# Kernel tuning notes

Hardware: AMD Instinct MI355X
Metric: run time of the kernel (lower is better)

The kernel has to match this reference:

```python
import jax, jax.numpy as jnp
import numpy as np

NUM_HEADS = 16
HEAD_DIM = 64
D_MODEL = NUM_HEADS * HEAD_DIM
DFF = 4096
LN_EPS = 1e-3  # keras LayerNormalization default epsilon


def layer_norm(x, gamma, beta):
    mu = jnp.mean(x, axis=-1, keepdims=True)
    var = jnp.mean(jnp.square(x - mu), axis=-1, keepdims=True)
    return (x - mu) * jax.lax.rsqrt(var + LN_EPS) * gamma + beta


def setup_inputs() -> dict:
    key = jax.random.key(0)
    ks = jax.random.split(key, 8)
    N, T = 2, 2048
    s = 0.02
    return {
        "x": jax.random.normal(ks[0], (N, T, D_MODEL), dtype=jnp.float32),
        "mask": jnp.ones((N, T), dtype=jnp.float32),
        "w_qkv": jax.random.normal(ks[1], (D_MODEL, 3 * D_MODEL), dtype=jnp.float32) * s,
        "b_qkv": jnp.zeros((3 * D_MODEL,), dtype=jnp.float32),
        "w_ff": jax.random.normal(ks[2], (D_MODEL, DFF), dtype=jnp.float32) * s,
        "b_ff": jnp.zeros((DFF,), dtype=jnp.float32),
        "w_out": jax.random.normal(ks[3], (DFF, D_MODEL), dtype=jnp.float32) * s,
        "b_out": jnp.zeros((D_MODEL,), dtype=jnp.float32),
        "ln1_g": jnp.ones((D_MODEL,), dtype=jnp.float32),
        "ln1_b": jnp.zeros((D_MODEL,), dtype=jnp.float32),
        "ln2_g": jnp.ones((D_MODEL,), dtype=jnp.float32),
        "ln2_b": jnp.zeros((D_MODEL,), dtype=jnp.float32),
    }


def reference(x, mask, w_qkv, b_qkv, w_ff, b_ff, w_out, b_out, ln1_g, ln1_b, ln2_g, ln2_b):
    N, T, _ = x.shape
    H, D = NUM_HEADS, HEAD_DIM
    # --- MHA ---
    qkv = x @ w_qkv + b_qkv                     # [N, T, 3*H*D]
    qkv = qkv.reshape(N, T, H, D, 3)
    qkv = jnp.transpose(qkv, (4, 0, 2, 1, 3))   # [3, N, H, T, D]
    q, k, v = qkv[0], qkv[1], qkv[2]
    logits = jnp.einsum('nhqd,nhkd->nhqk', q, k) * (1.0 / (D ** 0.5))
    # NB: faithful to original: mask[:, None, :, None] masks the QUERY axis
    logits = logits + (1.0 - mask[:, None, :, None]) * -1e9
    attn = jax.nn.softmax(logits, axis=-1)
    ctx = jnp.einsum('nhqk,nhkd->nhqd', attn, v)  # [N, H, T, D]
    ctx = jnp.transpose(ctx, (0, 2, 1, 3)).reshape(N, T, H * D)
    # dropout_rc1: identity (training=False)
    h = layer_norm(x + ctx, ln1_g, ln1_b)
    # --- FFN ---
    ff = jax.nn.relu(h @ w_ff + b_ff)             # [N, T, DFF]
    out = layer_norm(h + ff @ w_out + b_out, ln2_g, ln2_b)
    return out
```

## Files before the change

### kernel.cpp

```cpp
#include <hip/hip_runtime.h>
#include <hip/hip_fp8.h>
#include <stdint.h>

#define DM    1024
#define DFFN  4096
#define NTOK  4096
#define TT    2048
#define NHEAD 16
#define HD    64
#define LN_EPS 1e-3f
#define QSCALE 0.18033688011112042f

typedef float  f32x4  __attribute__((ext_vector_type(4)));
typedef __bf16 bf16x8 __attribute__((ext_vector_type(8)));
typedef long   lx2    __attribute__((ext_vector_type(2)));

using void_as1 = __attribute__((address_space(1))) void;
using void_as3 = __attribute__((address_space(3))) void;

__device__ __forceinline__ void g2l16(const void* g, void* l) {
    __builtin_amdgcn_global_load_lds((const void_as1*)g, (void_as3*)l, 16, 0, 0);
}

__device__ __forceinline__ unsigned short f2bf(float f) {
    unsigned u = __builtin_bit_cast(unsigned, f);
    u += 0x7FFFu + ((u >> 16) & 1u);
    return (unsigned short)(u >> 16);
}

__device__ __forceinline__ float bf2f(unsigned short u) {
    unsigned v = (unsigned)u << 16;
    return __builtin_bit_cast(float, v);
}

__device__ __forceinline__ float fexp2(float x) {
#if __has_builtin(__builtin_amdgcn_exp2f)
    return __builtin_amdgcn_exp2f(x);
#else
    return exp2f(x);
#endif
}

template <bool HI>
__device__ __forceinline__ unsigned cvt2fp8(float a, float b, unsigned old) {
#if __has_builtin(__builtin_amdgcn_cvt_pk_fp8_f32)
    return (unsigned)__builtin_amdgcn_cvt_pk_fp8_f32(a, b, (int)old, HI);
#else
    __hip_fp8_e4m3 ta(a), tb(b);
    unsigned w = (unsigned)ta.__x | ((unsigned)tb.__x << 8);
    return HI ? ((old & 0x0000FFFFu) | (w << 16)) : ((old & 0xFFFF0000u) | w);
#endif
}

__device__ __forceinline__ unsigned char f2fp8(float f) {
    return (unsigned char)(cvt2fp8<false>(f, 0.f, 0u) & 0xffu);
}

__global__ __launch_bounds__(256) void cast_fp8_kernel(
    const float* __restrict__ in, unsigned char* __restrict__ out, int n4) {
    int i = blockIdx.x * 256 + threadIdx.x;
    if (i < n4) {
        float4 v = ((const float4*)in)[i];
        unsigned p = cvt2fp8<false>(v.x, v.y, 0u);
        p = cvt2fp8<true>(v.z, v.w, p);
        ((unsigned*)out)[i] = p;
    }
}

__global__ __launch_bounds__(256) void transpose_cast_kernel(
    const float* __restrict__ w, unsigned short* __restrict__ wT, int K, int Nc) {
    __shared__ float tile[32][33];
    int tx = threadIdx.x & 31, ty = threadIdx.x >> 5;
    int n0 = blockIdx.x * 32, k0 = blockIdx.y * 32;
#pragma unroll
    for (int i = 0; i < 4; ++i)
        tile[ty + 8 * i][tx] = w[(size_t)(k0 + ty + 8 * i) * Nc + (n0 + tx)];
    __syncthreads();
#pragma unroll
    for (int i = 0; i < 4; ++i)
        wT[(size_t)(n0 + ty + 8 * i) * K + (k0 + tx)] = f2bf(tile[tx][ty + 8 * i]);
}

__global__ __launch_bounds__(256) void transpose_qkv_fp8_kernel(
    const float* __restrict__ w, unsigned char* __restrict__ wT) {
    __shared__ float tile[32][33];
    int tx = threadIdx.x & 31, ty = threadIdx.x >> 5;
    int c0 = blockIdx.x * 32, k0 = blockIdx.y * 32;
#pragma unroll
    for (int i = 0; i < 4; ++i)
        tile[ty + 8 * i][tx] = w[(size_t)(k0 + ty + 8 * i) * 3072 + (c0 + tx)];
    __syncthreads();
#pragma unroll
    for (int i = 0; i < 4; ++i) {
        const int col = c0 + ty + 8 * i;
        const int h = col / 192;
        const int rem = col - h * 192;
        const int d = rem / 3;
        const int s = rem - d * 3;
        const int colp = s * 1024 + h * 64 + d;
        wT[(size_t)colp * 1024 + (k0 + tx)] = f2fp8(tile[tx][ty + 8 * i]);
    }
}

__global__ __launch_bounds__(256, 4) void gemm_qkv_fp8_kernel(
    const unsigned char* __restrict__ A,
    const unsigned char* __restrict__ Bt,
    const float* __restrict__ bias,
    unsigned char* __restrict__ oq,
    unsigned char* __restrict__ ok,
    unsigned char* __restrict__ ov) {
    __shared__ __align__(16) unsigned char As[128 * 64];
    __shared__ __align__(16) unsigned char Bs[128 * 64];
    const int tid  = threadIdx.x;
    const int wave = tid >> 6, lane = tid & 63;
    const int quad = lane >> 4, l16 = lane & 15;
    const int sw2 = (l16 >> 1) & 3;
    const int wm = wave >> 1, wn = wave & 1;
    int fb = blockIdx.x + 24 * blockIdx.y;
    fb = (fb & 7) * 96 + (fb >> 3);
    const int nBase = (fb % 24) * 128, mBase = (fb / 24) * 128;

    f32x4 acc[4][4] = {};

    for (int k0 = 0; k0 < 1024; k0 += 64) {
#pragma unroll
        for (int i = 0; i < 2; ++i) {
            const int chunk = i * 256 + tid;
            const int row = chunk >> 2, p = chunk & 3;
            const int l = p ^ ((row >> 1) & 3);
            g2l16(A + (size_t)(mBase + row) * 1024 + (k0 + l * 16),
                  (char*)As + (size_t)(i * 256 + wave * 64) * 16);
        }
#pragma unroll
        for (int i = 0; i < 2; ++i) {
            const int chunk = i * 256 + tid;
            const int row = chunk >> 2, p = chunk & 3;
            const int l = p ^ ((row >> 1) & 3);
            g2l16(Bt + (size_t)(nBase + row) * 1024 + (k0 + l * 16),
                  (char*)Bs + (size_t)(i * 256 + wave * 64) * 16);
        }
        __syncthreads();
        lx2 af[4], bf[4];
#pragma unroll
        for (int i = 0; i < 4; ++i)
            af[i] = *(const lx2*)(const void*)(
                As + (wm * 64 + i * 16 + l16) * 64 + ((quad ^ sw2) << 4));
#pragma unroll
        for (int j = 0; j < 4; ++j)
            bf[j] = *(const lx2*)(const void*)(
                Bs + (wn * 64 + j * 16 + l16) * 64 + ((quad ^ sw2) << 4));
#pragma unroll
        for (int i = 0; i < 4; ++i)
#pragma unroll
            for (int j = 0; j < 4; ++j) {
                acc[i][j] = __builtin_amdgcn_mfma_f32_16x16x32_fp8_fp8(af[i].x, bf[j].x, acc[i][j], 0, 0, 0);
                acc[i][j] = __builtin_amdgcn_mfma_f32_16x16x32_fp8_fp8(af[i].y, bf[j].y, acc[i][j], 0, 0, 0);
            }
        __syncthreads();
    }

#pragma unroll
    for (int i = 0; i < 4; ++i) {
        const int rbase = mBase + wm * 64 + i * 16 + quad * 4;
#pragma unroll
        for (int j = 0; j < 4; ++j) {
            const int colp = nBase + wn * 64 + j * 16 + l16;
            const int s = colp >> 10;
            const int h = (colp >> 6) & 15;
            const int d = colp & 63;
            const float bv = bias[h * 192 + d * 3 + s];
#pragma unroll
            for (int r = 0; r < 4; ++r) {
                const int row = rbase + r;
                const float v = acc[i][j][r] + bv;
                const int n = row >> 11, t = row & (TT - 1);
                const int nh = n * NHEAD + h;
                if (s == 0)
                    oq[((size_t)nh * TT + t) * HD + d] = f2fp8(v * QSCALE);
                else if (s == 1)
                    ok[((size_t)nh * TT + t) * HD + d] = f2fp8(v);
                else {
                    const int tl = t & 127;
                    const int tp = ((tl & 15) << 3) | (tl >> 4);
                    ov[((size_t)nh * HD + d) * TT + (t & ~127) + tp] = f2fp8(v);
                }
            }
        }
    }
}

template <int EPI>
__global__ __launch_bounds__(256, 4) void gemm_bt_kernel(
    const unsigned short* __restrict__ A,
    const unsigned short* __restrict__ Bt,
    const float* __restrict__ bias,
    unsigned short* __restrict__ ob,
    unsigned short* __restrict__ ot0,
    unsigned short* __restrict__ ot1,
    unsigned short* __restrict__ ot2,
    unsigned short* __restrict__ ot3,
    int K, int Ksplit) {
    __shared__ unsigned short As[128 * 64];
    __shared__ unsigned short Bs[128 * 64];
    const int tid  = threadIdx.x;
    const int wave = tid >> 6, lane = tid & 63;
    const int quad = lane >> 4, l16 = lane & 15;
    const int sw = l16 & 7;
    const int wm = wave >> 1, wn = wave & 1;
    int fb = blockIdx.x + gridDim.x * blockIdx.y;
    const int cpx = (gridDim.x * gridDim.y) >> 3;
    fb = (fb & 7) * cpx + (fb >> 3);
    const int nBase = (fb % gridDim.x) * 128, mBase = (fb / gridDim.x) * 128;
    const int kb = blockIdx.z * Ksplit, ke = kb + Ksplit;

    f32x4 acc[4][4] = {};

    for (int k0 = kb; k0 < ke; k0 += 64) {
#pragma unroll
        for (int i = 0; i < 4; ++i) {
            const int chunk = i * 256 + tid;
            const int row = chunk >> 3, kc = chunk & 7;
            const int kl = kc ^ (row & 7);
            g2l16(A  + (size_t)(mBase + row) * K + (k0 + kl * 8),
                  (char*)As + (size_t)(i * 256 + wave * 64) * 16);
        }
#pragma unroll
        for (int i = 0; i < 4; ++i) {
            const int chunk = i * 256 + tid;
            const int row = chunk >> 3, kc = chunk & 7;
            const int kl = kc ^ (row & 7);
            g2l16(Bt + (size_t)(nBase + row) * K + (k0 + kl * 8),
                  (char*)Bs + (size_t)(i * 256 + wave * 64) * 16);
        }
        __syncthreads();
#pragma unroll
        for (int ks = 0; ks < 2; ++ks) {
            bf16x8 af[4], bfr[4];
#pragma unroll
            for (int i = 0; i < 4; ++i)
                af[i] = *(const bf16x8*)(const void*)(
                    As + (wm * 64 + i * 16 + l16) * 64 + (((ks * 4 + quad) ^ sw) << 3));
#pragma unroll
            for (int j = 0; j < 4; ++j)
                bfr[j] = *(const bf16x8*)(const void*)(
                    Bs + (wn * 64 + j * 16 + l16) * 64 + (((ks * 4 + quad) ^ sw) << 3));
#pragma unroll
            for (int i = 0; i < 4; ++i)
#pragma unroll
                for (int j = 0; j < 4; ++j)
                    acc[i][j] = __builtin_amdgcn_mfma_f32_16x16x32_bf16(af[i], bfr[j], acc[i][j], 0, 0, 0);
        }
        __syncthreads();
    }

    unsigned short* dst2 = nullptr;
    if (EPI == 2)
        dst2 = (blockIdx.z == 0) ? ot0 : (blockIdx.z == 1) ? ot1
             : (blockIdx.z == 2) ? ot2 : ot3;

#pragma unroll
    for (int i = 0; i < 4; ++i) {
        const int rbase = mBase + wm * 64 + i * 16 + quad * 4;
#pragma unroll
        for (int j = 0; j < 4; ++j) {
            const int col = nBase + wn * 64 + j * 16 + l16;
            const float bv = (EPI == 2) ? 0.0f : bias[col];
#pragma unroll
            for (int r = 0; r < 4; ++r) {
                const int row = rbase + r;
                const float v = acc[i][j][r] + bv;
                if (EPI == 1)
                    ob[(size_t)row * DFFN + col] = f2bf(fmaxf(v, 0.0f));
                else
                    dst2[(size_t)row * DM + col] = f2bf(v);
            }
        }
    }
}

__global__ __launch_bounds__(256, 4) void attn_kernel(
    const unsigned char* __restrict__ q,
    const unsigned char* __restrict__ k,
    const unsigned char* __restrict__ vt,
    unsigned short* __restrict__ ctx) {
    __shared__ __align__(16) unsigned char Ks[2][128 * 64];
    __shared__ __align__(16) unsigned char Vs[2][64 * 128];
    __shared__ __align__(16) unsigned char Plds[4][16 * 128];
    const int tid  = threadIdx.x;
    const int wave = tid >> 6, lane = tid & 63;
    const int quad = lane >> 4, l16 = lane & 15;
    const int sw2 = (l16 >> 1) & 3;
    const int sw3 = l16 & 7;
    const int nh = blockIdx.x & 31;
    const int qt = blockIdx.x >> 5;
    const unsigned char* qh = q  + (size_t)nh * TT * HD;
    const unsigned char* kh = k  + (size_t)nh * TT * HD;
    const unsigned char* vh = vt + (size_t)nh * HD * TT;

    const int qrow = qt * 64 + wave * 16;
    lx2 qa = *(const lx2*)(const void*)(
        qh + (size_t)(qrow + l16) * HD + quad * 16);

    f32x4 o[4] = {};
    f32x4 od = {};
    const long ONES8 = 0x3838383838383838L;
    unsigned char* pw = &Plds[wave][0];

    auto stageKV = [&](int b, int kt) {
#pragma unroll
        for (int i = 0; i < 2; ++i) {
            const int widx = i * 4 + wave;
            const int r = widx * 16 + (lane >> 2);
            const int lc = (lane & 3) ^ ((lane >> 3) & 3);
            g2l16(kh + (size_t)(kt + r) * HD + lc * 16,
                  (char*)&Ks[b][0] + widx * 1024);
        }
#pragma unroll
        for (int i = 0; i < 2; ++i) {
            const int widx = i * 4 + wave;
            const int d = widx * 8 + (lane >> 3);
            const int lc = (lane & 7) ^ ((lane >> 3) & 7);
            g2l16(vh + (size_t)d * TT + kt + lc * 16,
                  (char*)&Vs[b][0] + widx * 1024);
        }
    };

    stageKV(0, 0);

#pragma unroll 1
    for (int t = 0; t < TT / 128; ++t) {
        const int p = t & 1;
        if (t + 1 < TT / 128) {
            stageKV(p ^ 1, (t + 1) * 128);
            asm volatile("s_waitcnt vmcnt(4)" ::: "memory");
        } else {
            asm volatile("s_waitcnt vmcnt(0)" ::: "memory");
        }
        __builtin_amdgcn_s_barrier();

        f32x4 s[8];
#pragma unroll
        for (int c = 0; c < 8; ++c) {
            const int r = c * 16 + l16;
            const lx2 kb = *(const lx2*)(const void*)(
                &Ks[p][0] + r * 64 + ((quad ^ sw2) << 4));
            f32x4 z = {};
            z = __builtin_amdgcn_mfma_f32_16x16x32_fp8_fp8(qa.x, kb.x, z, 0, 0, 0);
            s[c] = __builtin_amdgcn_mfma_f32_16x16x32_fp8_fp8(qa.y, kb.y, s[c] = z, 0, 0, 0);
        }
#pragma unroll
        for (int c = 0; c < 8; ++c)
#pragma unroll
            for (int r = 0; r < 4; ++r)
                s[c][r] = fexp2(s[c][r]);
#pragma unroll
        for (int r = 0; r < 4; ++r) {
            const int row = quad * 4 + r;
            const int physc = (l16 >> 1) ^ (row & 7);
            unsigned lo = cvt2fp8<false>(s[0][r], s[1][r], 0u);
            lo = cvt2fp8<true>(s[2][r], s[3][r], lo);
            unsigned hi = cvt2fp8<false>(s[4][r], s[5][r], 0u);
            hi = cvt2fp8<true>(s[6][r], s[7][r], hi);
            uint2 wv; wv.x = lo; wv.y = hi;
            *(uint2*)(void*)(pw + row * 128 + physc * 16 + ((l16 & 1) << 3)) = wv;
        }
        asm volatile("s_waitcnt lgkmcnt(0)" ::: "memory");
#pragma unroll
        for (int m = 0; m < 2; ++m) {
            const lx2 pa = *(const lx2*)(const void*)(
                pw + l16 * 128 + (((m * 4 + quad) ^ sw3) << 4));
#pragma unroll
            for (int dc = 0; dc < 4; ++dc) {
                const lx2 vb = *(const lx2*)(const void*)(
                    &Vs[p][0] + (dc * 16 + l16) * 128 + (((m * 4 + quad) ^ sw3) << 4));
                o[dc] = __builtin_amdgcn_mfma_f32_16x16x32_fp8_fp8(pa.x, vb.x, o[dc], 0, 0, 0);
                o[dc] = __builtin_amdgcn_mfma_f32_16x16x32_fp8_fp8(pa.y, vb.y, o[dc], 0, 0, 0);
            }
            od = __builtin_amdgcn_mfma_f32_16x16x32_fp8_fp8(pa.x, ONES8, od, 0, 0, 0);
            od = __builtin_amdgcn_mfma_f32_16x16x32_fp8_fp8(pa.y, ONES8, od, 0, 0, 0);
        }
        __builtin_amdgcn_sched_barrier(0);
        __builtin_amdgcn_s_barrier();
    }

    const int n = nh >> 4, h = nh & 15;
#pragma unroll
    for (int r = 0; r < 4; ++r) {
        const float inv = 1.0f / od[r];
        const int trow = qrow + quad * 4 + r;
        unsigned short* op = ctx + ((size_t)(n * TT + trow)) * DM + h * HD;
#pragma unroll
        for (int dc = 0; dc < 4; ++dc)
            op[dc * 16 + l16] = f2bf(o[dc][r] * inv);
    }
}

template <int MODE>
__global__ __launch_bounds__(256) void add_ln_kernel(
    const float* __restrict__ af, const unsigned short* __restrict__ ab,
    const unsigned short* __restrict__ bb, const unsigned short* __restrict__ cb,
    const unsigned short* __restrict__ db, const unsigned short* __restrict__ eb,
    const float* __restrict__ cbias,
    const float* __restrict__ gamma, const float* __restrict__ beta,
    float* __restrict__ outf, unsigned short* __restrict__ outb) {
    const int row = blockIdx.x;
    const int tid = threadIdx.x;
    const int lane = tid & 63, wave = tid >> 6;
    float4 x;
    if (MODE == 1) {
        const float4 av = ((const float4*)(af + (size_t)row * DM))[tid];
        const ushort4 bv = ((const ushort4*)(ab + (size_t)row * DM))[tid];
        x.x = av.x + bf2f(bv.x); x.y = av.y + bf2f(bv.y);
        x.z = av.z + bf2f(bv.z); x.w = av.w + bf2f(bv.w);
    } else {
        const ushort4 av = ((const ushort4*)(ab + (size_t)row * DM))[tid];
        const ushort4 bv = ((const ushort4*)(bb + (size_t)row * DM))[tid];
        const ushort4 cv = ((const ushort4*)(cb + (size_t)row * DM))[tid];
        const ushort4 dv = ((const ushort4*)(db + (size_t)row * DM))[tid];
        const ushort4 ev = ((const ushort4*)(eb + (size_t)row * DM))[tid];
        const float4 c4 = ((const float4*)cbias)[tid];
        x.x = bf2f(av.x) + bf2f(bv.x) + bf2f(cv.x) + bf2f(dv.x) + bf2f(ev.x) + c4.x;
        x.y = bf2f(av.y) + bf2f(bv.y) + bf2f(cv.y) + bf2f(dv.y) + bf2f(ev.y) + c4.y;
        x.z = bf2f(av.z) + bf2f(bv.z) + bf2f(cv.z) + bf2f(dv.z) + bf2f(ev.z) + c4.z;
        x.w = bf2f(av.w) + bf2f(bv.w) + bf2f(cv.w) + bf2f(dv.w) + bf2f(ev.w) + c4.w;
    }
    float s = x.x + x.y + x.z + x.w;
    float q = x.x * x.x + x.y * x.y + x.z * x.z + x.w * x.w;
#pragma unroll
    for (int off = 1; off < 64; off <<= 1) {
        s += __shfl_xor(s, off, 64);
        q += __shfl_xor(q, off, 64);
    }
    __shared__ float sh[8];
    if (lane == 0) { sh[wave] = s; sh[4 + wave] = q; }
    __syncthreads();
    s = sh[0] + sh[1] + sh[2] + sh[3];
    q = sh[4] + sh[5] + sh[6] + sh[7];
    const float mu = s * (1.0f / DM);
    const float var = q * (1.0f / DM) - mu * mu;
    const float rstd = rsqrtf(var + LN_EPS);
    const float4 g4 = ((const float4*)gamma)[tid];
    const float4 b4 = ((const float4*)beta)[tid];
    float4 o;
    o.x = (x.x - mu) * rstd * g4.x + b4.x;
    o.y = (x.y - mu) * rstd * g4.y + b4.y;
    o.z = (x.z - mu) * rstd * g4.z + b4.z;
    o.w = (x.w - mu) * rstd * g4.w + b4.w;
    if (MODE == 1) {
        ushort4 ob;
        ob.x = f2bf(o.x); ob.y = f2bf(o.y); ob.z = f2bf(o.z); ob.w = f2bf(o.w);
        ((ushort4*)(outb + (size_t)row * DM))[tid] = ob;
    } else {
        ((float4*)(outf + (size_t)row * DM))[tid] = o;
    }
}

extern "C" void kernel_launch(void* const* d_in, const int* in_sizes, int n_in,
                              void* d_out, int out_size, void* d_ws, size_t ws_size,
                              hipStream_t stream) {
    const float* x     = (const float*)d_in[0];
    const float* w_qkv = (const float*)d_in[2];
    const float* b_qkv = (const float*)d_in[3];
    const float* w_ff  = (const float*)d_in[4];
    const float* b_ff  = (const float*)d_in[5];
    const float* w_out = (const float*)d_in[6];
    const float* b_out = (const float*)d_in[7];
    const float* ln1_g = (const float*)d_in[8];
    const float* ln1_b = (const float*)d_in[9];
    const float* ln2_g = (const float*)d_in[10];
    const float* ln2_b = (const float*)d_in[11];

    char* ws = (char*)d_ws;
    unsigned char*  x8    = (unsigned char*)(ws);
    unsigned char*  wq8   = (unsigned char*)(ws + 8388608);
    unsigned short* wffT  = (unsigned short*)(ws + 14680064);
    unsigned short* woutT = (unsigned short*)(ws + 23068672);
    unsigned char*  qb    = (unsigned char*)(ws + 31457280);
    unsigned char*  kb    = (unsigned char*)(ws + 39845888);
    unsigned char*  vtb   = (unsigned char*)(ws + 48234496);
    unsigned short* ctxb  = (unsigned short*)(ws + 56623104);
    unsigned short* pt2   = (unsigned short*)(ws + 65011712);
    unsigned short* pt3   = (unsigned short*)(ws + 73400320);
    unsigned short* hb    = (unsigned short*)(ws + 90177536);
    unsigned short* ffb   = (unsigned short*)(ws + 98566144);
    unsigned short* pt0   = (unsigned short*)(ws + 132120576);
    unsigned short* pt1   = (unsigned short*)(ws + 140509184);

    cast_fp8_kernel<<<(NTOK * DM / 4 + 255) / 256, 256, 0, stream>>>(x, x8, NTOK * DM / 4);
    transpose_qkv_fp8_kernel<<<dim3(3072 / 32, DM / 32), 256, 0, stream>>>(w_qkv, wq8);
    transpose_cast_kernel<<<dim3(DFFN / 32, DM / 32), 256, 0, stream>>>(w_ff, wffT, DM, DFFN);
    transpose_cast_kernel<<<dim3(DM / 32, DFFN / 32), 256, 0, stream>>>(w_out, woutT, DFFN, DM);

    gemm_qkv_fp8_kernel<<<dim3(3072 / 128, NTOK / 128), 256, 0, stream>>>(
        x8, wq8, b_qkv, qb, kb, vtb);

    attn_kernel<<<1024, 256, 0, stream>>>(qb, kb, vtb, ctxb);

    add_ln_kernel<1><<<NTOK, 256, 0, stream>>>(x, ctxb, nullptr, nullptr, nullptr,
                                               nullptr, nullptr,
                                               ln1_g, ln1_b, nullptr, hb);

    gemm_bt_kernel<1><<<dim3(DFFN / 128, NTOK / 128), 256, 0, stream>>>(
        hb, wffT, b_ff, ffb, nullptr, nullptr, nullptr, nullptr, DM, DM);

    gemm_bt_kernel<2><<<dim3(DM / 128, NTOK / 128, 4), 256, 0, stream>>>(
        ffb, woutT, nullptr, nullptr, pt0, pt1, pt2, pt3, DFFN, DFFN / 4);

    add_ln_kernel<2><<<NTOK, 256, 0, stream>>>(nullptr, hb, pt0, pt1, pt2, pt3,
                                               b_out,
                                               ln2_g, ln2_b, (float*)d_out, nullptr);
}
```

Measured before the change: 295.5 us.

## Add 256x256-tile bf16 GEMM with half-K pipelining for the FFN up-projection

Replaces the 128x128-tile GEMM for the first FFN layer (h @ w_ff + bias, relu) with a new 512-thread kernel computing 256x256 output tiles. Each K-step of 64 is split into two 32-wide halves, with a double-buffered LDS pipeline, s_setprio around the MFMA bursts, and an XCD-aware block remap. The goal is more operand reuse per LDS byte and better overlap of global loads with MFMA. In exchange it needs heavy register use (8x4 accumulators per wave) and a 1-block-per-XCD-chunk grid of only 256 blocks, which may hurt occupancy and tail balance.

```diff
diff --git a/kernel.cpp b/kernel.cpp
--- a/kernel.cpp
+++ b/kernel.cpp
@@ -273,6 +273,123 @@
                     ob[(size_t)row * DFFN + col] = f2bf(fmaxf(v, 0.0f));
                 else
                     dst2[(size_t)row * DM + col] = f2bf(v);
+            }
+        }
+    }
+}
+
+#define MFMA_HALF(h) \
+    _Pragma("unroll") \
+    for (int mf2 = 0; mf2 < 4; ++mf2) { \
+        _Pragma("unroll") \
+        for (int nf = 0; nf < 4; ++nf) \
+            acc[((h) & 1) * 4 + mf2][nf] = __builtin_amdgcn_mfma_f32_16x16x32_bf16( \
+                a[mf2], b[nf], acc[((h) & 1) * 4 + mf2][nf], 0, 0, 0); \
+    }
+
+#define PHASE_TAIL(h) \
+    __builtin_amdgcn_s_barrier(); \
+    asm volatile("s_waitcnt lgkmcnt(0)" ::: "memory"); \
+    __builtin_amdgcn_s_setprio(1); \
+    MFMA_HALF(h) \
+    __builtin_amdgcn_s_setprio(0); \
+    __builtin_amdgcn_s_barrier();
+
+__global__ __launch_bounds__(512, 2) void gemm_bt_256_kernel(
+    const unsigned short* __restrict__ A,
+    const unsigned short* __restrict__ Bt,
+    const float* __restrict__ bias,
+    unsigned short* __restrict__ ob, int K) {
+    __shared__ __align__(16) unsigned short As[2][2][8192];
+    __shared__ __align__(16) unsigned short Bs[2][2][8192];
+    const int tid  = threadIdx.x;
+    const int wave = tid >> 6, lane = tid & 63;
+    const int quad = lane >> 4, l16 = lane & 15;
+    const int sw2 = (l16 >> 1) & 3;
+    const int wm = wave >> 2, wn = wave & 3;
+    const int aoff = (quad ^ sw2) << 3;
+    int bid = (int)blockIdx.x;
+    bid = (bid & 7) * 32 + (bid >> 3);
+    const int nBase = (bid & 15) * 256, mBase = (bid >> 4) * 256;
+    const int NT = K >> 6;
+    const unsigned short* Ab = A  + (size_t)mBase * K;
+    const unsigned short* Bb = Bt + (size_t)nBase * K;
+
+    f32x4 acc[8][4] = {};
+
+    auto stage = [&](const unsigned short* G, unsigned short* slot, int kOff) {
+#pragma unroll
+        for (int i = 0; i < 2; ++i) {
+            const int row = i * 128 + (tid >> 2);
+            const int l = (tid & 3) ^ ((row >> 1) & 3);
+            g2l16(G + (size_t)row * K + (kOff + l * 8),
+                  (char*)slot + (size_t)(i * 512 + wave * 64) * 16);
+        }
+    };
+
+    stage(Ab, &As[0][0][0], 0);
+    stage(Bb, &Bs[0][0][0], 0);
+    stage(Ab, &As[0][1][0], 32);
+    stage(Bb, &Bs[0][1][0], 32);
+    stage(Ab, &As[1][0][0], 64);
+    stage(Bb, &Bs[1][0][0], 64);
+    asm volatile("s_waitcnt vmcnt(4)" ::: "memory");
+    __builtin_amdgcn_s_barrier();
+
+#pragma unroll 1
+    for (int t = 0; t < NT; ++t) {
+        const int p = t & 1;
+        const int t1 = (t + 1) & (NT - 1);
+        const int t2 = (t + 2) & (NT - 1);
+        bf16x8 a[4], b[4];
+        stage(Ab, &As[p ^ 1][1][0], t1 * 64 + 32);
+        stage(Bb, &Bs[p ^ 1][1][0], t1 * 64 + 32);
+#pragma unroll
+        for (int mf = 0; mf < 4; ++mf)
+            a[mf] = *(const bf16x8*)(const void*)(
+                &As[p][0][(wm * 128 + mf * 16 + l16) * 32 + aoff]);
+#pragma unroll
+        for (int nf = 0; nf < 4; ++nf)
+            b[nf] = *(const bf16x8*)(const void*)(
+                &Bs[p][0][(wn * 64 + nf * 16 + l16) * 32 + aoff]);
+        PHASE_TAIL(0)
+        asm volatile("s_waitcnt vmcnt(8)" ::: "memory");
+#pragma unroll
+        for (int mf = 0; mf < 4; ++mf)
+            a[mf] = *(const bf16x8*)(const void*)(
+                &As[p][0][(wm * 128 + (4 + mf) * 16 + l16) * 32 + aoff]);
+        PHASE_TAIL(1)
+        stage(Ab, &As[p][0][0], t2 * 64);
+        stage(Bb, &Bs[p][0][0], t2 * 64);
+#pragma unroll
+        for (int mf = 0; mf < 4; ++mf)
+            a[mf] = *(const bf16x8*)(const void*)(
+                &As[p][1][(wm * 128 + mf * 16 + l16) * 32 + aoff]);
+#pragma unroll
+        for (int nf = 0; nf < 4; ++nf)
+            b[nf] = *(const bf16x8*)(const void*)(
+                &Bs[p][1][(wn * 64 + nf * 16 + l16) * 32 + aoff]);
+        PHASE_TAIL(2)
+        asm volatile("s_waitcnt vmcnt(8)" ::: "memory");
+#pragma unroll
+        for (int mf = 0; mf < 4; ++mf)
+            a[mf] = *(const bf16x8*)(const void*)(
+                &As[p][1][(wm * 128 + (4 + mf) * 16 + l16) * 32 + aoff]);
+        PHASE_TAIL(3)
+    }
+    asm volatile("s_waitcnt vmcnt(0)" ::: "memory");
+
+#pragma unroll
+    for (int mf = 0; mf < 8; ++mf) {
+        const int rbase = mBase + wm * 128 + mf * 16 + quad * 4;
+#pragma unroll
+        for (int nf = 0; nf < 4; ++nf) {
+            const int col = nBase + wn * 64 + nf * 16 + l16;
+            const float bv = bias[col];
+#pragma unroll
+            for (int r = 0; r < 4; ++r) {
+                const float v = acc[mf][nf][r] + bv;
+                ob[(size_t)(rbase + r) * DFFN + col] = f2bf(fmaxf(v, 0.0f));
             }
         }
     }
@@ -500,8 +617,7 @@
                                                nullptr, nullptr,
                                                ln1_g, ln1_b, nullptr, hb);
 
-    gemm_bt_kernel<1><<<dim3(DFFN / 128, NTOK / 128), 256, 0, stream>>>(
-        hb, wffT, b_ff, ffb, nullptr, nullptr, nullptr, nullptr, DM, DM);
+    gemm_bt_256_kernel<<<256, 512, 0, stream>>>(hb, wffT, b_ff, ffb, DM);
 
     gemm_bt_kernel<2><<<dim3(DM / 128, NTOK / 128, 4), 256, 0, stream>>>(
         ffb, woutT, nullptr, nullptr, pt0, pt1, pt2, pt3, DFFN, DFFN / 4);
```

New measurement: 310.2 us. +5.0%, slower.
